# Optimization experiments

Hardware: AMD Instinct MI355X
Metric: run time of the kernel (lower is better)

The kernel has to match this reference:

```python
import jax, jax.numpy as jnp
import numpy as np

# Deformable DETR encoder layer constants (match init_kwargs / input_specs)
SPATIAL_SHAPES = [(100, 152), (50, 76), (25, 38), (13, 19)]  # (H, W) per level
D_MODEL, D_FFN = 256, 1024
N_LEVELS, N_HEADS, N_POINTS = 4, 8, 4
HEAD_DIM = D_MODEL // N_HEADS
LEN_IN = sum(h * w for h, w in SPATIAL_SHAPES)  # 20197
BATCH = 2


def layer_norm(x, g, b, eps=1e-5):
    m = x.mean(-1, keepdims=True)
    v = ((x - m) ** 2).mean(-1, keepdims=True)
    return (x - m) * jax.lax.rsqrt(v + eps) * g + b


def sample_level(value_l, loc, H, W):
    # value_l: [B, nH, H*W, d]; loc: [B, nH, N, 2] normalized to [0,1]
    # Bilinear sampling, align_corners=False, zero padding (torch grid_sample semantics)
    x = loc[..., 0] * W - 0.5
    y = loc[..., 1] * H - 0.5
    x0, y0 = jnp.floor(x), jnp.floor(y)
    out = jnp.zeros(loc.shape[:-1] + (value_l.shape[-1],), value_l.dtype)
    for dx, dy in ((0, 0), (1, 0), (0, 1), (1, 1)):
        xi, yi = x0 + dx, y0 + dy
        w = (1.0 - jnp.abs(x - xi)) * (1.0 - jnp.abs(y - yi))
        valid = (xi >= 0) & (xi < W) & (yi >= 0) & (yi < H)
        idx = (jnp.clip(yi, 0, H - 1) * W + jnp.clip(xi, 0, W - 1)).astype(jnp.int32)
        v = jnp.take_along_axis(value_l, idx[..., None], axis=2)  # [B,nH,N,d]
        out = out + v * (w * valid.astype(value_l.dtype))[..., None]
    return out


def ms_deform_attn(query, src, ref, W_off, b_off, W_attn, b_attn, W_val, b_val, W_out, b_out):
    B, Lq, C = query.shape
    # value projection -> [B, nH, Len_in, head_dim]
    value = (src @ W_val + b_val).reshape(B, LEN_IN, N_HEADS, HEAD_DIM).transpose(0, 2, 1, 3)
    off = (query @ W_off + b_off).reshape(B, Lq, N_HEADS, N_LEVELS, N_POINTS, 2)
    attn = (query @ W_attn + b_attn).reshape(B, Lq, N_HEADS, N_LEVELS * N_POINTS)
    attn = jax.nn.softmax(attn, -1).reshape(B, Lq, N_HEADS, N_LEVELS, N_POINTS)
    # offset normalizer is (W, H) per level
    normalizer = jnp.array([[w, h] for h, w in SPATIAL_SHAPES], dtype=query.dtype)
    loc = ref[:, :, None, :, None, :] + off / normalizer[None, None, None, :, None, :]  # [B,Lq,nH,nL,nP,2]
    out = jnp.zeros((B, N_HEADS, Lq, HEAD_DIM), query.dtype)
    start = 0
    for l, (H, W) in enumerate(SPATIAL_SHAPES):
        v_l = value[:, :, start:start + H * W]
        start += H * W
        loc_l = loc[:, :, :, l].transpose(0, 2, 1, 3, 4).reshape(B, N_HEADS, Lq * N_POINTS, 2)
        s = sample_level(v_l, loc_l, H, W).reshape(B, N_HEADS, Lq, N_POINTS, HEAD_DIM)
        a = attn[:, :, :, l].transpose(0, 2, 1, 3)  # [B,nH,Lq,nP]
        out = out + (s * a[..., None]).sum(3)
    out = out.transpose(0, 2, 1, 3).reshape(B, Lq, C)
    return out @ W_out + b_out


def setup_inputs() -> dict:
    key = jax.random.key(0)
    ks = jax.random.split(key, 20)
    s = 0.02
    spatial_shapes = jnp.array(SPATIAL_SHAPES, dtype=jnp.int64)
    lsi = np.cumsum([0] + [h * w for h, w in SPATIAL_SHAPES[:-1]])
    return {
        'src': jax.random.normal(ks[0], (BATCH, LEN_IN, D_MODEL), jnp.float32),
        'pos': jax.random.normal(ks[1], (BATCH, LEN_IN, D_MODEL), jnp.float32),
        'reference_points': jax.random.uniform(ks[2], (BATCH, LEN_IN, N_LEVELS, 2), jnp.float32),
        'spatial_shapes': spatial_shapes,
        'level_start_index': jnp.array(lsi, dtype=jnp.int64),
        'W_off': jax.random.normal(ks[3], (D_MODEL, N_HEADS * N_LEVELS * N_POINTS * 2), jnp.float32) * s,
        'b_off': jax.random.normal(ks[4], (N_HEADS * N_LEVELS * N_POINTS * 2,), jnp.float32) * s,
        'W_attn': jax.random.normal(ks[5], (D_MODEL, N_HEADS * N_LEVELS * N_POINTS), jnp.float32) * s,
        'b_attn': jnp.zeros((N_HEADS * N_LEVELS * N_POINTS,), jnp.float32),
        'W_val': jax.random.normal(ks[6], (D_MODEL, D_MODEL), jnp.float32) * s,
        'b_val': jnp.zeros((D_MODEL,), jnp.float32),
        'W_out': jax.random.normal(ks[7], (D_MODEL, D_MODEL), jnp.float32) * s,
        'b_out': jnp.zeros((D_MODEL,), jnp.float32),
        'W1': jax.random.normal(ks[8], (D_MODEL, D_FFN), jnp.float32) * s,
        'b1': jnp.zeros((D_FFN,), jnp.float32),
        'W2': jax.random.normal(ks[9], (D_FFN, D_MODEL), jnp.float32) * s,
        'b2': jnp.zeros((D_MODEL,), jnp.float32),
        'g1': jnp.ones((D_MODEL,), jnp.float32),
        'be1': jnp.zeros((D_MODEL,), jnp.float32),
        'g2': jnp.ones((D_MODEL,), jnp.float32),
        'be2': jnp.zeros((D_MODEL,), jnp.float32),
    }


def reference(src, pos, reference_points, spatial_shapes, level_start_index,
              W_off, b_off, W_attn, b_attn, W_val, b_val, W_out, b_out,
              W1, b1, W2, b2, g1, be1, g2, be2):
    # eval mode: all dropouts are identity; ReLUDropout -> relu
    query = src + pos
    src2 = ms_deform_attn(query, src, reference_points,
                          W_off, b_off, W_attn, b_attn, W_val, b_val, W_out, b_out)
    x = layer_norm(src + src2, g1, be1)
    ffn = jax.nn.relu(x @ W1 + b1) @ W2 + b2
    return layer_norm(x + ffn, g2, be2)
```

## Files before the change

### kernel.cpp

```cpp
#include <hip/hip_runtime.h>
#include <math.h>

#define LEN_IN_C 20197
#define BATCH_C 2
#define BL_C (BATCH_C * LEN_IN_C)

typedef short  bf16x8 __attribute__((ext_vector_type(8)));
typedef float  f32x4  __attribute__((ext_vector_type(4)));

__device__ __forceinline__ ushort f2bf(float f) {
    unsigned u = __float_as_uint(f);
    return (ushort)((u + 0x7fffu + ((u >> 16) & 1u)) >> 16);
}
__device__ __forceinline__ float bf2f(ushort u) {
    return __uint_as_float((uint)u << 16);
}
__device__ __forceinline__ uint pkbf(float a, float b) {
    uint r;
    asm("v_cvt_pk_bf16_f32 %0, %1, %2" : "=v"(r) : "v"(a), "v"(b));
    return r;
}
__device__ __forceinline__ void dot2bf(float& a, uint v, uint w) {
    asm("v_dot2_f32_bf16 %0, %1, %2, %0" : "+v"(a) : "v"(v), "v"(w));
}
__device__ __forceinline__ void gload16(const void* g, void* l) {
    __builtin_amdgcn_global_load_lds(
        (const __attribute__((address_space(1))) unsigned char*)g,
        (__attribute__((address_space(3))) unsigned char*)l, 16, 0, 0);
}
__device__ __forceinline__ int xcd_swz(int lid, int nwg) {
    const int q = nwg >> 3, r = nwg & 7;
    const int xcd = lid & 7, p = lid >> 3;
    return (xcd < r ? xcd * (q + 1) : r * (q + 1) + (xcd - r) * q) + p;
}

__device__ __forceinline__ void tcast32(
    const float* W, ushort* WT, int K, int N, int n0, int k0, float* tile )
{
    const int ty = threadIdx.x >> 3, tx = threadIdx.x & 7;
    float4 v = *(const float4*)(W + (size_t)(k0 + ty) * N + n0 + tx * 4);
    tile[ty * 33 + tx * 4 + 0] = v.x; tile[ty * 33 + tx * 4 + 1] = v.y;
    tile[ty * 33 + tx * 4 + 2] = v.z; tile[ty * 33 + tx * 4 + 3] = v.w;
    __syncthreads();
    ushort4 o;
    o.x = f2bf(tile[(tx * 4 + 0) * 33 + ty]);
    o.y = f2bf(tile[(tx * 4 + 1) * 33 + ty]);
    o.z = f2bf(tile[(tx * 4 + 2) * 33 + ty]);
    o.w = f2bf(tile[(tx * 4 + 3) * 33 + ty]);
    *(ushort4*)(WT + (size_t)(n0 + ty) * K + k0 + tx * 4) = o;
}

__global__ __launch_bounds__(256) void prep_all(
    const float* __restrict__ src, const float* __restrict__ pos,
    const float* __restrict__ Wv, const float* __restrict__ Wo,
    const float* __restrict__ Wa, const float* __restrict__ Wout,
    const float* __restrict__ W1, const float* __restrict__ W2,
    const float* __restrict__ bo, const float* __restrict__ ba,
    ushort* __restrict__ Tval, ushort* __restrict__ Toa,
    ushort* __restrict__ Tout, ushort* __restrict__ TW1,
    ushort* __restrict__ TW2, float* __restrict__ boa,
    ushort* __restrict__ qout, ushort* __restrict__ srcb)
{
    __shared__ float tile[32 * 33];
    const int bx = blockIdx.x;
    const int tid = threadIdx.x;
    if (bx < 64) {
        tcast32(Wv, Tval, 256, 256, (bx & 7) * 32, (bx >> 3) * 32, tile);
    } else if (bx < 128) {
        const int s = bx - 64;
        tcast32(Wout, Tout, 256, 256, (s & 7) * 32, (s >> 3) * 32, tile);
    } else if (bx < 384) {
        const int s = bx - 128;
        tcast32(W1, TW1, 256, 1024, (s & 31) * 32, (s >> 5) * 32, tile);
    } else if (bx < 640) {
        const int s = bx - 384;
        tcast32(W2, TW2, 1024, 256, (s & 7) * 32, (s >> 3) * 32, tile);
    } else if (bx < 736) {
        const int idx = (bx - 640) * 256 + tid;
        const int n = idx >> 6, k4 = (idx & 63) * 4;
        ushort4 o; ushort* po = (ushort*)&o;
        #pragma unroll
        for (int j = 0; j < 4; ++j) {
            const int k = k4 + j;
            const float v = (n < 256) ? Wo[(size_t)k * 256 + n]
                                      : Wa[(size_t)k * 128 + (n - 256)];
            po[j] = f2bf(v);
        }
        *(ushort4*)(Toa + (size_t)n * 256 + k4) = o;
    } else if (bx < 738) {
        const int n = (bx - 736) * 256 + tid;
        if (n < 384) boa[n] = (n < 256) ? bo[n] : ba[n - 256];
    } else {
        const int n8 = BL_C * 32;
        for (int i = (bx - 738) * 256 + tid; i < n8; i += 1024 * 256) {
            const size_t base = (size_t)i * 8;
            float4 a0 = *(const float4*)(src + base);
            float4 a1 = *(const float4*)(src + base + 4);
            float4 b0 = *(const float4*)(pos + base);
            float4 b1 = *(const float4*)(pos + base + 4);
            uint4 o;
            o.x = pkbf(a0.x + b0.x, a0.y + b0.y);
            o.y = pkbf(a0.z + b0.z, a0.w + b0.w);
            o.z = pkbf(a1.x + b1.x, a1.y + b1.y);
            o.w = pkbf(a1.z + b1.z, a1.w + b1.w);
            *(uint4*)(qout + base) = o;
            uint4 s4;
            s4.x = pkbf(a0.x, a0.y); s4.y = pkbf(a0.z, a0.w);
            s4.z = pkbf(a1.x, a1.y); s4.w = pkbf(a1.z, a1.w);
            *(uint4*)(srcb + base) = s4;
        }
    }
}

template <bool RELU>
__device__ __forceinline__ void gemm_core(
    ushort* lsB,
    const int lid,
    const ushort* __restrict__ A, const ushort* __restrict__ BT,
    const float* __restrict__ bias, ushort* __restrict__ C,
    const int M, const int N, const int K, const int NT, const int nwg)
{
    const int nid = xcd_swz(lid, nwg);
    const int nt = nid % NT, mt = nid / NT;
    const int row0 = mt * 128, col0 = nt * 128;

    const int tid = threadIdx.x;
    const int ln = tid & 63, wv = tid >> 6;
    const int l16 = ln & 15, lk = ln >> 4;

    uint abase[2];
    #pragma unroll
    for (int m = 0; m < 2; ++m) {
        int rr = row0 + wv * 32 + m * 16 + l16;
        if (rr > M - 1) rr = M - 1;
        abase[m] = (uint)rr * K + lk * 8;
    }
    uint bbase[8], bxor[8];
    #pragma unroll
    for (int n = 0; n < 8; ++n) {
        const int brow = n * 16 + l16;
        bbase[n] = (uint)(brow * 256 + lk * 16);
        bxor[n]  = (uint)((brow & 7) << 4);
    }

    f32x4 acc[2][8] = {};
    const int nch = K >> 7;

    for (int ch = 0; ch < nch; ++ch) {
        const int kc0 = ch << 7;

        bf16x8 ar[4][2];
        #pragma unroll
        for (int s = 0; s < 4; ++s)
            #pragma unroll
            for (int m = 0; m < 2; ++m)
                ar[s][m] = *(const bf16x8*)(A + abase[m] + kc0 + s * 32);

        if (ch) __syncthreads();
        #pragma unroll
        for (int j = 0; j < 8; ++j) {
            const int d = j * 256 + tid;
            const int brow = d >> 4;
            const int c = (d & 15) ^ (brow & 7);
            gload16(BT + (size_t)(col0 + brow) * K + kc0 + c * 8,
                    (char*)lsB + j * 4096 + wv * 1024);
        }
        __syncthreads();

        #pragma unroll
        for (int gs = 0; gs < 4; ++gs) {
            bf16x8 bv[8];
            #pragma unroll
            for (int n = 0; n < 8; ++n)
                bv[n] = *(const bf16x8*)((const char*)lsB +
                        ((bbase[n] + gs * 64) ^ bxor[n]));
            #pragma unroll
            for (int m = 0; m < 2; ++m)
                #pragma unroll
                for (int n = 0; n < 8; ++n)
                    acc[m][n] = __builtin_amdgcn_mfma_f32_16x16x32_bf16(
                        bv[n], ar[gs][m], acc[m][n], 0, 0, 0);
        }
    }

    #pragma unroll
    for (int m = 0; m < 2; ++m) {
        const int grow = row0 + wv * 32 + m * 16 + l16;
        if (grow >= M) continue;
        ushort* crow = C + (size_t)grow * N;
        #pragma unroll
        for (int n = 0; n < 8; ++n) {
            const int col4 = col0 + n * 16 + lk * 4;
            float4 bs = *(const float4*)(bias + col4);
            f32x4 v = acc[m][n];
            float o0 = v[0] + bs.x, o1 = v[1] + bs.y, o2 = v[2] + bs.z, o3 = v[3] + bs.w;
            if (RELU) {
                o0 = fmaxf(o0, 0.f); o1 = fmaxf(o1, 0.f);
                o2 = fmaxf(o2, 0.f); o3 = fmaxf(o3, 0.f);
            }
            *(uint2*)(crow + col4) = make_uint2(pkbf(o0, o1), pkbf(o2, o3));
        }
    }
}

template <bool RELU>
__global__ __launch_bounds__(256) void gemm_bs(
    const ushort* __restrict__ A, const ushort* __restrict__ BT,
    const float* __restrict__ bias, ushort* __restrict__ C,
    const int M, const int N, const int K, const int NT, const int nwg)
{
    __shared__ ushort lsB[128 * 128];
    gemm_core<RELU>(lsB, blockIdx.x, A, BT, bias, C, M, N, K, NT, nwg);
}

__global__ __launch_bounds__(256) void gemm_dual(
    const ushort* __restrict__ A1, const ushort* __restrict__ BT1,
    const float* __restrict__ b1, ushort* __restrict__ C1,
    const int N1, const int NT1, const int nwg1,
    const ushort* __restrict__ A2, const ushort* __restrict__ BT2,
    const float* __restrict__ b2, ushort* __restrict__ C2,
    const int N2, const int NT2, const int nwg2)
{
    __shared__ ushort lsB[128 * 128];
    if ((int)blockIdx.x < nwg1)
        gemm_core<false>(lsB, blockIdx.x, A1, BT1, b1, C1, BL_C, N1, 256, NT1, nwg1);
    else
        gemm_core<false>(lsB, blockIdx.x - nwg1, A2, BT2, b2, C2, BL_C, N2, 256, NT2, nwg2);
}

__global__ __launch_bounds__(256) void sample_kernel(
    const ushort* __restrict__ value,
    const ushort* __restrict__ oa,
    const float* __restrict__ ref,
    ushort* __restrict__ outbf)
{
    constexpr int Hs[4] = {100, 50, 25, 13};
    constexpr int Ws[4] = {152, 76, 38, 19};
    constexpr int St[4] = {0, 15200, 19000, 19950};
    constexpr int NWG = (BL_C + 7) / 8;

    const int bq0 = xcd_swz(blockIdx.x, NWG) * 8;
    const int t = threadIdx.x;

    __shared__ uint2 s_pw[8][8][33];

    #pragma unroll
    for (int rnd = 0; rnd < 4; ++rnd) {
        const int qi2 = t >> 7, r2 = t & 127;
        const int qloc = rnd * 2 + qi2;
        int bq = bq0 + qloc; if (bq > BL_C - 1) bq = BL_C - 1;
        const int b = (bq >= LEN_IN_C) ? 1 : 0;
        const int h = r2 >> 4, i = r2 & 15, l = i >> 2, p = i & 3;
        const ushort* crow = oa + (size_t)bq * 384;

        float lg = bf2f(crow[256 + h * 16 + i]);
        float mx = lg;
        #pragma unroll
        for (int o = 1; o < 16; o <<= 1) mx = fmaxf(mx, __shfl_xor(mx, o, 16));
        float e = __expf(lg - mx), sm = e;
        #pragma unroll
        for (int o = 1; o < 16; o <<= 1) sm += __shfl_xor(sm, o, 16);
        const float aw = e / sm;

        const uint ov = *(const uint*)(crow + h * 32 + l * 8 + p * 2);
        const float ox = __uint_as_float(ov << 16);
        const float oy = __uint_as_float(ov & 0xffff0000u);
        const float2 rxy = *(const float2*)(ref + (size_t)bq * 8 + l * 2);
        const int H = Hs[l], W = Ws[l];
        const float x = rxy.x * (float)W + ox - 0.5f;
        const float y = rxy.y * (float)H + oy - 0.5f;
        const float x0f = floorf(x), y0f = floorf(y);
        const float fx = x - x0f, fy = y - y0f;
        const int x0 = (int)x0f, y0 = (int)y0f;

        const float wx0 = (x0 >= 0 && x0 < W) ? (1.f - fx) : 0.f;
        const float wx1 = (x0 + 1 >= 0 && x0 + 1 < W) ? fx : 0.f;
        int xb = x0 < 0 ? 0 : (x0 > W - 2 ? W - 2 : x0);
        float wLx = (xb == x0) ? wx0 : ((xb == x0 + 1) ? wx1 : 0.f);
        float wRx = (xb + 1 == x0 + 1) ? wx1 : ((xb + 1 == x0) ? wx0 : 0.f);
        wLx *= aw; wRx *= aw;

        const uint rowb = (uint)(b * LEN_IN_C + St[l] + xb);
        #pragma unroll
        for (int dy = 0; dy < 2; ++dy) {
            const int yy = y0 + dy;
            const bool vy = (yy >= 0) & (yy < H);
            const float wy = vy ? (dy ? fy : 1.f - fy) : 0.f;
            const int yc = yy < 0 ? 0 : (yy > H - 1 ? H - 1 : yy);
            const uint off = (rowb + (uint)(yc * W)) * 512u;
            s_pw[qloc][h][i * 2 + dy] = make_uint2(off, pkbf(wRx * wy, wLx * wy));
        }
    }
    __syncthreads();

    const int q = t >> 5, h2 = (t >> 2) & 7, d4 = t & 3;
    int bq = bq0 + q; if (bq > BL_C - 1) bq = BL_C - 1;
    const char* vb = (const char*)value;
    const uint toff = (uint)(h2 * 64 + d4 * 16);

    float a0 = 0.f, a1 = 0.f, a2 = 0.f, a3 = 0.f;
    float a4 = 0.f, a5 = 0.f, a6 = 0.f, a7 = 0.f;
    #pragma unroll 4
    for (int j = 0; j < 32; ++j) {
        const uint2 pw = s_pw[q][h2][j];
        const char* p = vb + (size_t)(pw.x + toff);
        const uint4 v0 = *(const uint4*)p;
        const uint4 v1 = *(const uint4*)(p + 512);
        const uint w = pw.y;
        dot2bf(a0, __builtin_amdgcn_perm(v0.x, v1.x, 0x05040100u), w);
        dot2bf(a1, __builtin_amdgcn_perm(v0.x, v1.x, 0x07060302u), w);
        dot2bf(a2, __builtin_amdgcn_perm(v0.y, v1.y, 0x05040100u), w);
        dot2bf(a3, __builtin_amdgcn_perm(v0.y, v1.y, 0x07060302u), w);
        dot2bf(a4, __builtin_amdgcn_perm(v0.z, v1.z, 0x05040100u), w);
        dot2bf(a5, __builtin_amdgcn_perm(v0.z, v1.z, 0x07060302u), w);
        dot2bf(a6, __builtin_amdgcn_perm(v0.w, v1.w, 0x05040100u), w);
        dot2bf(a7, __builtin_amdgcn_perm(v0.w, v1.w, 0x07060302u), w);
    }
    uint4 o;
    o.x = pkbf(a0, a1); o.y = pkbf(a2, a3);
    o.z = pkbf(a4, a5); o.w = pkbf(a6, a7);
    *(uint4*)(outbf + (size_t)bq * 256 + h2 * 32 + d4 * 8) = o;
}

template <bool ABF, bool OF32>
__global__ __launch_bounds__(256) void add_ln(
    const void* __restrict__ ap, const ushort* __restrict__ bp,
    const float* __restrict__ g, const float* __restrict__ be,
    void* __restrict__ op)
{
    const int row = blockIdx.x * 4 + (threadIdx.x >> 6);
    if (row >= BL_C) return;
    const int ln = threadIdx.x & 63;
    const size_t base = (size_t)row * 256 + ln * 4;

    float x[4];
    if (ABF) {
        ushort4 a4 = *(const ushort4*)((const ushort*)ap + base);
        x[0] = bf2f(a4.x); x[1] = bf2f(a4.y); x[2] = bf2f(a4.z); x[3] = bf2f(a4.w);
    } else {
        float4 a4 = *(const float4*)((const float*)ap + base);
        x[0] = a4.x; x[1] = a4.y; x[2] = a4.z; x[3] = a4.w;
    }
    ushort4 b4 = *(const ushort4*)(bp + base);
    x[0] += bf2f(b4.x); x[1] += bf2f(b4.y); x[2] += bf2f(b4.z); x[3] += bf2f(b4.w);

    float s = x[0] + x[1] + x[2] + x[3];
    #pragma unroll
    for (int o = 32; o >= 1; o >>= 1) s += __shfl_xor(s, o, 64);
    const float mean = s * (1.f / 256.f);
    float d0 = x[0] - mean, d1 = x[1] - mean, d2 = x[2] - mean, d3 = x[3] - mean;
    float ss = d0 * d0 + d1 * d1 + d2 * d2 + d3 * d3;
    #pragma unroll
    for (int o = 32; o >= 1; o >>= 1) ss += __shfl_xor(ss, o, 64);
    const float rs = rsqrtf(ss * (1.f / 256.f) + 1e-5f);

    float4 gv = *(const float4*)(g + ln * 4);
    float4 bv = *(const float4*)(be + ln * 4);
    float o0 = d0 * rs * gv.x + bv.x;
    float o1 = d1 * rs * gv.y + bv.y;
    float o2 = d2 * rs * gv.z + bv.z;
    float o3 = d3 * rs * gv.w + bv.w;

    if (OF32) {
        *(float4*)((float*)op + base) = make_float4(o0, o1, o2, o3);
    } else {
        ushort4 st;
        st.x = f2bf(o0); st.y = f2bf(o1); st.z = f2bf(o2); st.w = f2bf(o3);
        *(ushort4*)((ushort*)op + base) = st;
    }
}

extern "C" void kernel_launch(void* const* d_in, const int* in_sizes, int n_in,
                              void* d_out, int out_size, void* d_ws, size_t ws_size,
                              hipStream_t stream) {
    const float* src    = (const float*)d_in[0];
    const float* pos    = (const float*)d_in[1];
    const float* refpts = (const float*)d_in[2];
    const float* W_off  = (const float*)d_in[5];
    const float* b_off  = (const float*)d_in[6];
    const float* W_attn = (const float*)d_in[7];
    const float* b_attn = (const float*)d_in[8];
    const float* W_val  = (const float*)d_in[9];
    const float* b_val  = (const float*)d_in[10];
    const float* W_out  = (const float*)d_in[11];
    const float* b_out  = (const float*)d_in[12];
    const float* W1     = (const float*)d_in[13];
    const float* b1     = (const float*)d_in[14];
    const float* W2     = (const float*)d_in[15];
    const float* b2     = (const float*)d_in[16];
    const float* g1     = (const float*)d_in[17];
    const float* be1    = (const float*)d_in[18];
    const float* g2     = (const float*)d_in[19];
    const float* be2    = (const float*)d_in[20];
    float* out = (float*)d_out;
    (void)in_sizes; (void)n_in; (void)out_size; (void)ws_size;

    const int BL = BL_C;
    char* ws = (char*)d_ws;
    const size_t HB  = (size_t)BL * 256 * 2;
    const size_t OAB = (size_t)BL * 384 * 2;

    ushort* q_bf    = (ushort*)(ws);
    ushort* x_bf    = (ushort*)(ws);
    ushort* val_bf  = (ushort*)(ws + HB);
    ushort* oa_bf   = (ushort*)(ws + 2 * HB);
    ushort* ao_bf   = (ushort*)(ws + 2 * HB + OAB);
    ushort* src2_bf = (ushort*)(ws + 3 * HB + OAB);
    ushort* srcb_bf = (ushort*)(ws + 4 * HB + OAB);
    ushort* ffn2_bf = srcb_bf;
    ushort* mid_bf  = val_bf;
    char*   wts     = ws + 5 * HB + OAB;
    ushort* Tval = (ushort*)(wts);
    ushort* Toa  = Tval + 256 * 256;
    ushort* Tout = Toa + 384 * 256;
    ushort* TW1  = Tout + 256 * 256;
    ushort* TW2  = TW1 + 1024 * 256;
    float*  boa  = (float*)(TW2 + 256 * 1024);

    dim3 blk(256);
    const int MT = (BL + 127) / 128;

    prep_all<<<dim3(738 + 1024), blk, 0, stream>>>(
        src, pos, W_val, W_off, W_attn, W_out, W1, W2, b_off, b_attn,
        Tval, Toa, Tout, TW1, TW2, boa, q_bf, srcb_bf);

    gemm_dual<<<dim3(MT * 2 + MT * 3), blk, 0, stream>>>(
        srcb_bf, Tval, b_val, val_bf, 256, 2, MT * 2,
        q_bf, Toa, boa, oa_bf, 384, 3, MT * 3);

    sample_kernel<<<dim3((BL + 7) / 8), blk, 0, stream>>>(val_bf, oa_bf, refpts, ao_bf);

    gemm_bs<false><<<dim3(MT * 2), blk, 0, stream>>>(
        ao_bf, Tout, b_out, src2_bf, BL, 256, 256, 2, MT * 2);

    add_ln<true, false><<<dim3((BL + 3) / 4), blk, 0, stream>>>(
        srcb_bf, src2_bf, g1, be1, x_bf);

    gemm_bs<true><<<dim3(MT * 8), blk, 0, stream>>>(
        x_bf, TW1, b1, mid_bf, BL, 1024, 256, 8, MT * 8);

    gemm_bs<false><<<dim3(MT * 2), blk, 0, stream>>>(
        mid_bf, TW2, b2, ffn2_bf, BL, 256, 1024, 2, MT * 2);

    add_ln<true, true><<<dim3((BL + 3) / 4), blk, 0, stream>>>(
        x_bf, ffn2_bf, g2, be2, out);
}
```

Baseline: 266.1 us.

## Add persistent K=256 GEMM keeping full weight tile in LDS across row tiles

Introduces a persistent GEMM kernel for the K=256 projections. It loads the full 128x256 weight tile into LDS once, keeps the A fragments in registers, and loops over several M tiles per workgroup, prefetching the next A rows while the current tile is written out. It is used for the value/offset dual GEMM (2 tiles per block), the output projection, and the FFN1 GEMM (4 tiles per block), which removes repeated B-tile staging and the K-loop synchronisation. The change also raises the sample-loop unroll from 4 to 8. In exchange it doubles LDS per block, raises register pressure, and hardcodes grid sizes (158/316/79) that assume MT=316.

```diff
diff --git a/kernel.cpp b/kernel.cpp
--- a/kernel.cpp
+++ b/kernel.cpp
@@ -112,15 +112,146 @@
     }
 }
 
-template <bool RELU>
-__device__ __forceinline__ void gemm_core(
+template <int L, bool RELU>
+__device__ __forceinline__ void gemm_pers_core(
     ushort* lsB,
     const int lid,
     const ushort* __restrict__ A, const ushort* __restrict__ BT,
     const float* __restrict__ bias, ushort* __restrict__ C,
+    const int M, const int N, const int NT, const int P, const int nwg)
+{
+    const int nid = xcd_swz(lid, nwg);
+    const int nt = nid % NT, p0 = nid / NT;
+    const int col0 = nt * 128;
+
+    const int tid = threadIdx.x;
+    const int ln = tid & 63, wv = tid >> 6;
+    const int l16 = ln & 15, lk = ln >> 4;
+
+    #pragma unroll
+    for (int j = 0; j < 16; ++j) {
+        const int d = j * 256 + tid;
+        const int brow = d >> 5;
+        const int c = (d & 31) ^ (brow & 7);
+        gload16(BT + (size_t)(col0 + brow) * 256 + c * 8,
+                (char*)lsB + j * 4096 + wv * 1024);
+    }
+
+    uint bbase[8], bxor[8];
+    #pragma unroll
+    for (int n = 0; n < 8; ++n) {
+        const int brow = n * 16 + l16;
+        bbase[n] = (uint)(brow * 512 + lk * 16);
+        bxor[n]  = (uint)((brow & 7) << 4);
+    }
+
+    bf16x8 ar[8][2];
+    {
+        const int row0 = p0 * 128;
+        #pragma unroll
+        for (int s = 0; s < 8; ++s)
+            #pragma unroll
+            for (int m = 0; m < 2; ++m) {
+                int rr = row0 + wv * 32 + m * 16 + l16;
+                if (rr > M - 1) rr = M - 1;
+                ar[s][m] = *(const bf16x8*)(A + (uint)rr * 256 + lk * 8 + s * 32);
+            }
+    }
+    __syncthreads();
+
+    float4 bias4[8];
+    #pragma unroll
+    for (int n = 0; n < 8; ++n)
+        bias4[n] = *(const float4*)(bias + col0 + n * 16 + lk * 4);
+
+    #pragma unroll
+    for (int i = 0; i < L; ++i) {
+        const int mt = p0 + i * P;
+        const int row0 = mt * 128;
+
+        f32x4 acc[2][8] = {};
+        #pragma unroll
+        for (int gs = 0; gs < 8; ++gs) {
+            bf16x8 bv[8];
+            #pragma unroll
+            for (int n = 0; n < 8; ++n)
+                bv[n] = *(const bf16x8*)((const char*)lsB +
+                        ((bbase[n] + gs * 64) ^ bxor[n]));
+            #pragma unroll
+            for (int m = 0; m < 2; ++m)
+                #pragma unroll
+                for (int n = 0; n < 8; ++n)
+                    acc[m][n] = __builtin_amdgcn_mfma_f32_16x16x32_bf16(
+                        bv[n], ar[gs][m], acc[m][n], 0, 0, 0);
+        }
+
+        if (i + 1 < L) {
+            const int nrow0 = (mt + P) * 128;
+            #pragma unroll
+            for (int s = 0; s < 8; ++s)
+                #pragma unroll
+                for (int m = 0; m < 2; ++m) {
+                    int rr = nrow0 + wv * 32 + m * 16 + l16;
+                    if (rr > M - 1) rr = M - 1;
+                    ar[s][m] = *(const bf16x8*)(A + (uint)rr * 256 + lk * 8 + s * 32);
+                }
+        }
+
+        #pragma unroll
+        for (int m = 0; m < 2; ++m) {
+            const int grow = row0 + wv * 32 + m * 16 + l16;
+            if (grow >= M) continue;
+            ushort* crow = C + (size_t)grow * N;
+            #pragma unroll
+            for (int n = 0; n < 8; ++n) {
+                const int col4 = col0 + n * 16 + lk * 4;
+                f32x4 v = acc[m][n];
+                float o0 = v[0] + bias4[n].x, o1 = v[1] + bias4[n].y;
+                float o2 = v[2] + bias4[n].z, o3 = v[3] + bias4[n].w;
+                if (RELU) {
+                    o0 = fmaxf(o0, 0.f); o1 = fmaxf(o1, 0.f);
+                    o2 = fmaxf(o2, 0.f); o3 = fmaxf(o3, 0.f);
+                }
+                *(uint2*)(crow + col4) = make_uint2(pkbf(o0, o1), pkbf(o2, o3));
+            }
+        }
+    }
+}
+
+template <int L, bool RELU>
+__global__ __launch_bounds__(256) void gemm_pers(
+    const ushort* __restrict__ A, const ushort* __restrict__ BT,
+    const float* __restrict__ bias, ushort* __restrict__ C,
+    const int M, const int N, const int NT, const int P, const int nwg)
+{
+    __shared__ ushort lsB[128 * 256];
+    gemm_pers_core<L, RELU>(lsB, blockIdx.x, A, BT, bias, C, M, N, NT, P, nwg);
+}
+
+__global__ __launch_bounds__(256) void gemm_dual(
+    const ushort* __restrict__ A1, const ushort* __restrict__ BT1,
+    const float* __restrict__ b1, ushort* __restrict__ C1,
+    const int N1, const int NT1, const int P1, const int nwg1,
+    const ushort* __restrict__ A2, const ushort* __restrict__ BT2,
+    const float* __restrict__ b2, ushort* __restrict__ C2,
+    const int N2, const int NT2, const int P2, const int nwg2)
+{
+    __shared__ ushort lsB[128 * 256];
+    if ((int)blockIdx.x < nwg1)
+        gemm_pers_core<2, false>(lsB, blockIdx.x, A1, BT1, b1, C1, BL_C, N1, NT1, P1, nwg1);
+    else
+        gemm_pers_core<2, false>(lsB, blockIdx.x - nwg1, A2, BT2, b2, C2, BL_C, N2, NT2, P2, nwg2);
+}
+
+template <bool RELU>
+__global__ __launch_bounds__(256) void gemm_bs(
+    const ushort* __restrict__ A, const ushort* __restrict__ BT,
+    const float* __restrict__ bias, ushort* __restrict__ C,
     const int M, const int N, const int K, const int NT, const int nwg)
 {
-    const int nid = xcd_swz(lid, nwg);
+    __shared__ ushort lsB[128 * 128];
+
+    const int nid = xcd_swz(blockIdx.x, nwg);
     const int nt = nid % NT, mt = nid / NT;
     const int row0 = mt * 128, col0 = nt * 128;
 
@@ -203,31 +334,6 @@
     }
 }
 
-template <bool RELU>
-__global__ __launch_bounds__(256) void gemm_bs(
-    const ushort* __restrict__ A, const ushort* __restrict__ BT,
-    const float* __restrict__ bias, ushort* __restrict__ C,
-    const int M, const int N, const int K, const int NT, const int nwg)
-{
-    __shared__ ushort lsB[128 * 128];
-    gemm_core<RELU>(lsB, blockIdx.x, A, BT, bias, C, M, N, K, NT, nwg);
-}
-
-__global__ __launch_bounds__(256) void gemm_dual(
-    const ushort* __restrict__ A1, const ushort* __restrict__ BT1,
-    const float* __restrict__ b1, ushort* __restrict__ C1,
-    const int N1, const int NT1, const int nwg1,
-    const ushort* __restrict__ A2, const ushort* __restrict__ BT2,
-    const float* __restrict__ b2, ushort* __restrict__ C2,
-    const int N2, const int NT2, const int nwg2)
-{
-    __shared__ ushort lsB[128 * 128];
-    if ((int)blockIdx.x < nwg1)
-        gemm_core<false>(lsB, blockIdx.x, A1, BT1, b1, C1, BL_C, N1, 256, NT1, nwg1);
-    else
-        gemm_core<false>(lsB, blockIdx.x - nwg1, A2, BT2, b2, C2, BL_C, N2, 256, NT2, nwg2);
-}
-
 __global__ __launch_bounds__(256) void sample_kernel(
     const ushort* __restrict__ value,
     const ushort* __restrict__ oa,
@@ -300,7 +406,7 @@
 
     float a0 = 0.f, a1 = 0.f, a2 = 0.f, a3 = 0.f;
     float a4 = 0.f, a5 = 0.f, a6 = 0.f, a7 = 0.f;
-    #pragma unroll 4
+    #pragma unroll 8
     for (int j = 0; j < 32; ++j) {
         const uint2 pw = s_pw[q][h2][j];
         const char* p = vb + (size_t)(pw.x + toff);
@@ -424,20 +530,20 @@
         src, pos, W_val, W_off, W_attn, W_out, W1, W2, b_off, b_attn,
         Tval, Toa, Tout, TW1, TW2, boa, q_bf, srcb_bf);
 
-    gemm_dual<<<dim3(MT * 2 + MT * 3), blk, 0, stream>>>(
-        srcb_bf, Tval, b_val, val_bf, 256, 2, MT * 2,
-        q_bf, Toa, boa, oa_bf, 384, 3, MT * 3);
+    gemm_dual<<<dim3(2 * 158 + 3 * 158), blk, 0, stream>>>(
+        srcb_bf, Tval, b_val, val_bf, 256, 2, 158, 2 * 158,
+        q_bf, Toa, boa, oa_bf, 384, 3, 158, 3 * 158);
 
     sample_kernel<<<dim3((BL + 7) / 8), blk, 0, stream>>>(val_bf, oa_bf, refpts, ao_bf);
 
-    gemm_bs<false><<<dim3(MT * 2), blk, 0, stream>>>(
-        ao_bf, Tout, b_out, src2_bf, BL, 256, 256, 2, MT * 2);
+    gemm_pers<1, false><<<dim3(2 * 316), blk, 0, stream>>>(
+        ao_bf, Tout, b_out, src2_bf, BL, 256, 2, 316, 2 * 316);
 
     add_ln<true, false><<<dim3((BL + 3) / 4), blk, 0, stream>>>(
         srcb_bf, src2_bf, g1, be1, x_bf);
 
-    gemm_bs<true><<<dim3(MT * 8), blk, 0, stream>>>(
-        x_bf, TW1, b1, mid_bf, BL, 1024, 256, 8, MT * 8);
+    gemm_pers<4, true><<<dim3(8 * 79), blk, 0, stream>>>(
+        x_bf, TW1, b1, mid_bf, BL, 1024, 8, 79, 8 * 79);
 
     gemm_bs<false><<<dim3(MT * 2), blk, 0, stream>>>(
         mid_bf, TW2, b2, ffn2_bf, BL, 256, 1024, 2, MT * 2);
```

Measured after the change: 271.1 us. About the same (+1.8%).
